# Kernel optimization log

Measured on AMD Instinct MI355X. Metric: run time of the kernel, lower is better.

## Reference

```python
import jax, jax.numpy as jnp
import numpy as np

B, S, E, L = 4, 4096, 64, 3
INIT_SCALE = 0.03


def setup_inputs() -> dict:
    key = jax.random.key(0)
    ks = jax.random.split(key, 7)
    return {
        "x": jax.random.normal(ks[0], (B, S, S + 1), dtype=jnp.float32),
        "q_ws": jax.random.normal(ks[1], (L, E, E), dtype=jnp.float32) * INIT_SCALE,
        "k_ws": jax.random.normal(ks[2], (L, E, E), dtype=jnp.float32) * INIT_SCALE,
        "v_ws": jax.random.normal(ks[3], (L, E, E), dtype=jnp.float32) * INIT_SCALE,
        "random_matrix": jax.random.normal(ks[4], (S, E - 1), dtype=jnp.float32) * INIT_SCALE,
        "coeffs_attended": jax.random.normal(ks[5], (S, E), dtype=jnp.float32) * INIT_SCALE,
        "offset": jax.random.normal(ks[6], (1,), dtype=jnp.float32),
    }


def reference(x, q_ws, k_ws, v_ws, random_matrix, coeffs_attended, offset):
    seq_length = random_matrix.shape[0]
    # project first seq_length feature columns, keep the last column raw -> [B, S, E]
    av = jnp.concatenate(
        [jnp.einsum('bsf,fe->bse', x[:, :, :seq_length], random_matrix), x[:, :, -1:]],
        axis=2,
    )

    def layer(av, ws):
        qw, kw, vw = ws
        q = jnp.einsum('bse,ed->bsd', av, qw)   # [B, S, E]
        k = jnp.einsum('bse,ed->bsd', av, kw)
        v = jnp.einsum('bse,ed->bsd', av, vw)
        scores = jax.nn.softmax(jnp.einsum('bqd,bkd->bqk', q, k), axis=-1)  # [B, S, S]
        out = jnp.einsum('bqk,bkd->bqd', scores, v)
        # skip_connections=False: output replaces attended values
        return out, None

    av, _ = jax.lax.scan(layer, av, (q_ws, k_ws, v_ws))
    final = jnp.einsum('bij,ij->b', av, coeffs_attended)  # [B]
    return final + offset[0]
```

## Files before the change

kernel.cpp:

```cpp
#include <hip/hip_runtime.h>

#define SEQ  4096
#define EMB  64
#define NB   4
#define XROW 4097

typedef unsigned short ushort_t;
typedef __attribute__((ext_vector_type(8))) short short8;
typedef __attribute__((ext_vector_type(4))) float floatx4;

__device__ __forceinline__ ushort_t f2bf(float f) {
    union { float f; unsigned int u; } v; v.f = f;
    unsigned int r = v.u + 0x7FFFu + ((v.u >> 16) & 1u);
    return (ushort_t)(r >> 16);
}

__global__ __launch_bounds__(256) void prep_rmt(const float* __restrict__ rm,
                                                ushort_t* __restrict__ rmT) {
    int o = (blockIdx.x * 256 + threadIdx.x) * 4;
    int e = o >> 12;
    int f = o & 4095;
    alignas(8) ushort_t t[4];
    t[0] = f2bf((e < 63) ? rm[(size_t)(f + 0) * 63 + e] : 0.f);
    t[1] = f2bf((e < 63) ? rm[(size_t)(f + 1) * 63 + e] : 0.f);
    t[2] = f2bf((e < 63) ? rm[(size_t)(f + 2) * 63 + e] : 0.f);
    t[3] = f2bf((e < 63) ? rm[(size_t)(f + 3) * 63 + e] : 0.f);
    *(uint2*)&rmT[o] = *(uint2*)t;
}

__global__ __launch_bounds__(256) void proj_mfma(const float* __restrict__ x,
        const ushort_t* __restrict__ rmT, float* __restrict__ av) {
    __shared__ ushort_t xs[64 * 64];
    __shared__ ushort_t rs[64 * 64];
    const int tid = threadIdx.x;
    const int row0 = blockIdx.x * 64;
    const int w = tid >> 6, l = tid & 63;
    const int srow = tid >> 2, sc = (tid & 3) * 16;

    floatx4 acc[4];
    #pragma unroll
    for (int i = 0; i < 4; ++i) acc[i] = (floatx4){0.f, 0.f, 0.f, 0.f};

    float px[16];
    short8 pr0, pr1;
    {
        const float* xp = x + (size_t)(row0 + srow) * XROW + sc;
        #pragma unroll
        for (int i = 0; i < 16; ++i) px[i] = xp[i];
        const ushort_t* rp = rmT + (size_t)srow * SEQ + sc;
        pr0 = *(const short8*)&rp[0];
        pr1 = *(const short8*)&rp[8];
    }

    for (int k0 = 0; k0 < SEQ; k0 += 64) {
        __syncthreads();
        {
            alignas(16) ushort_t tmp[16];
            #pragma unroll
            for (int i = 0; i < 16; ++i) tmp[i] = f2bf(px[i]);
            *(short8*)&xs[srow * 64 + sc]     = *(short8*)&tmp[0];
            *(short8*)&xs[srow * 64 + sc + 8] = *(short8*)&tmp[8];
            *(short8*)&rs[srow * 64 + sc]     = pr0;
            *(short8*)&rs[srow * 64 + sc + 8] = pr1;
        }
        __syncthreads();
        if (k0 + 64 < SEQ) {
            const float* xp = x + (size_t)(row0 + srow) * XROW + (k0 + 64) + sc;
            #pragma unroll
            for (int i = 0; i < 16; ++i) px[i] = xp[i];
            const ushort_t* rp = rmT + (size_t)srow * SEQ + (k0 + 64) + sc;
            pr0 = *(const short8*)&rp[0];
            pr1 = *(const short8*)&rp[8];
        }
        #pragma unroll
        for (int ksp = 0; ksp < 2; ++ksp) {
            short8 a = *(short8*)&xs[(w * 16 + (l & 15)) * 64 + ksp * 32 + (l >> 4) * 8];
            #pragma unroll
            for (int nt = 0; nt < 4; ++nt) {
                short8 bf = *(short8*)&rs[(nt * 16 + (l & 15)) * 64 + ksp * 32 + (l >> 4) * 8];
                acc[nt] = __builtin_amdgcn_mfma_f32_16x16x32_bf16(a, bf, acc[nt], 0, 0, 0);
            }
        }
    }
    #pragma unroll
    for (int nt = 0; nt < 4; ++nt)
        #pragma unroll
        for (int r = 0; r < 4; ++r) {
            int row = row0 + w * 16 + (l >> 4) * 4 + r;
            int col = nt * 16 + (l & 15);
            float v = acc[nt][r];
            if (col == 63) v = x[(size_t)row * XROW + SEQ];
            av[(size_t)row * EMB + col] = v;
        }
}

__global__ __launch_bounds__(256) void qkv_mfma(const float* __restrict__ av,
        const float* __restrict__ qw, const float* __restrict__ kw,
        const float* __restrict__ vw, ushort_t* __restrict__ Qb,
        ushort_t* __restrict__ Kb, ushort_t* __restrict__ Vt) {
    __shared__ ushort_t avs[64 * 64];
    __shared__ ushort_t wqs[64 * 64], wks[64 * 64], wvs[64 * 64];
    const int tid = threadIdx.x;
    const int row0 = blockIdx.x * 64;
    const int w = tid >> 6, l = tid & 63;
    const int srow = tid >> 2, sc = (tid & 3) * 16;

    {
        const float* ap = av + (size_t)(row0 + srow) * EMB + sc;
        alignas(16) ushort_t tmp[16];
        #pragma unroll
        for (int i = 0; i < 16; ++i) tmp[i] = f2bf(ap[i]);
        *(short8*)&avs[srow * 64 + sc]     = *(short8*)&tmp[0];
        *(short8*)&avs[srow * 64 + sc + 8] = *(short8*)&tmp[8];
    }
    {
        alignas(16) ushort_t tq[16], tk[16], tv[16];
        #pragma unroll
        for (int i = 0; i < 16; ++i) {
            int kk = sc + i;
            tq[i] = f2bf(qw[kk * 64 + srow]);
            tk[i] = f2bf(kw[kk * 64 + srow]);
            tv[i] = f2bf(vw[kk * 64 + srow]);
        }
        *(short8*)&wqs[srow * 64 + sc]     = *(short8*)&tq[0];
        *(short8*)&wqs[srow * 64 + sc + 8] = *(short8*)&tq[8];
        *(short8*)&wks[srow * 64 + sc]     = *(short8*)&tk[0];
        *(short8*)&wks[srow * 64 + sc + 8] = *(short8*)&tk[8];
        *(short8*)&wvs[srow * 64 + sc]     = *(short8*)&tv[0];
        *(short8*)&wvs[srow * 64 + sc + 8] = *(short8*)&tv[8];
    }
    __syncthreads();

    floatx4 aq[4], ak[4], avv[4];
    #pragma unroll
    for (int i = 0; i < 4; ++i) {
        aq[i] = (floatx4){0.f, 0.f, 0.f, 0.f};
        ak[i] = aq[i]; avv[i] = aq[i];
    }
    #pragma unroll
    for (int ksp = 0; ksp < 2; ++ksp) {
        short8 a = *(short8*)&avs[(w * 16 + (l & 15)) * 64 + ksp * 32 + (l >> 4) * 8];
        #pragma unroll
        for (int nt = 0; nt < 4; ++nt) {
            int bo = (nt * 16 + (l & 15)) * 64 + ksp * 32 + (l >> 4) * 8;
            aq[nt]  = __builtin_amdgcn_mfma_f32_16x16x32_bf16(a, *(short8*)&wqs[bo], aq[nt], 0, 0, 0);
            ak[nt]  = __builtin_amdgcn_mfma_f32_16x16x32_bf16(a, *(short8*)&wks[bo], ak[nt], 0, 0, 0);
            avv[nt] = __builtin_amdgcn_mfma_f32_16x16x32_bf16(a, *(short8*)&wvs[bo], avv[nt], 0, 0, 0);
        }
    }

    const int b = row0 >> 12;
    #pragma unroll
    for (int nt = 0; nt < 4; ++nt)
        #pragma unroll
        for (int r = 0; r < 4; ++r) {
            int row = row0 + w * 16 + (l >> 4) * 4 + r;
            int col = nt * 16 + (l & 15);
            size_t o = (size_t)row * EMB + col;
            Qb[o] = f2bf(aq[nt][r]);
            Kb[o] = f2bf(ak[nt][r]);
            Vt[((size_t)b * EMB + col) * SEQ + (row & 4095)] = f2bf(avv[nt][r]);
        }
}

__global__ __launch_bounds__(256) void flash_mfma(const ushort_t* __restrict__ Qb,
        const ushort_t* __restrict__ Kb, const ushort_t* __restrict__ Vt,
        float* __restrict__ out) {
    __shared__ ushort_t ks[64 * 64];
    __shared__ ushort_t vt[64 * 64];
    __shared__ ushort_t ps[4][16 * 64];
    const int tid = threadIdx.x;
    const int w = tid >> 6, l = tid & 63;
    const int b = blockIdx.y;
    const int q0 = blockIdx.x * 64;
    const size_t base  = (size_t)b * SEQ * EMB;
    const size_t vbase = (size_t)b * EMB * SEQ;
    const int srow = tid >> 2, sc = (tid & 3) * 16;

    short8 qf[2];
    #pragma unroll
    for (int ksp = 0; ksp < 2; ++ksp)
        qf[ksp] = *(const short8*)&Qb[base + (size_t)(q0 + w * 16 + (l & 15)) * EMB
                                      + ksp * 32 + (l >> 4) * 8];

    short8 pk0, pk1, pv0, pv1;
    {
        const ushort_t* kp = Kb + base + (size_t)srow * EMB + sc;
        pk0 = *(const short8*)kp;
        pk1 = *(const short8*)(kp + 8);
        const ushort_t* vp = Vt + vbase + (size_t)srow * SEQ + sc;
        pv0 = *(const short8*)vp;
        pv1 = *(const short8*)(vp + 8);
    }

    floatx4 o_acc[4];
    #pragma unroll
    for (int i = 0; i < 4; ++i) o_acc[i] = (floatx4){0.f, 0.f, 0.f, 0.f};
    float lpart[4] = {0.f, 0.f, 0.f, 0.f};

    for (int kt = 0; kt < SEQ; kt += 64) {
        __syncthreads();
        *(short8*)&ks[srow * 64 + sc]     = pk0;
        *(short8*)&ks[srow * 64 + sc + 8] = pk1;
        *(short8*)&vt[srow * 64 + sc]     = pv0;
        *(short8*)&vt[srow * 64 + sc + 8] = pv1;
        __syncthreads();
        if (kt + 64 < SEQ) {
            const ushort_t* kp = Kb + base + (size_t)(kt + 64 + srow) * EMB + sc;
            pk0 = *(const short8*)kp;
            pk1 = *(const short8*)(kp + 8);
            const ushort_t* vp = Vt + vbase + (size_t)srow * SEQ + (kt + 64) + sc;
            pv0 = *(const short8*)vp;
            pv1 = *(const short8*)(vp + 8);
        }

        floatx4 s[4];
        #pragma unroll
        for (int nt = 0; nt < 4; ++nt) s[nt] = (floatx4){0.f, 0.f, 0.f, 0.f};
        #pragma unroll
        for (int ksp = 0; ksp < 2; ++ksp)
            #pragma unroll
            for (int nt = 0; nt < 4; ++nt) {
                short8 bf = *(short8*)&ks[(nt * 16 + (l & 15)) * 64 + ksp * 32 + (l >> 4) * 8];
                s[nt] = __builtin_amdgcn_mfma_f32_16x16x32_bf16(qf[ksp], bf, s[nt], 0, 0, 0);
            }

        #pragma unroll
        for (int nt = 0; nt < 4; ++nt)
            #pragma unroll
            for (int r = 0; r < 4; ++r) {
                float p = __expf(s[nt][r]);
                lpart[r] += p;
                ps[w][((l >> 4) * 4 + r) * 64 + nt * 16 + (l & 15)] = f2bf(p);
            }
        asm volatile("s_waitcnt lgkmcnt(0)" ::: "memory");

        #pragma unroll
        for (int ksp = 0; ksp < 2; ++ksp) {
            short8 af = *(short8*)&ps[w][(l & 15) * 64 + ksp * 32 + (l >> 4) * 8];
            #pragma unroll
            for (int nt = 0; nt < 4; ++nt) {
                short8 bf = *(short8*)&vt[(nt * 16 + (l & 15)) * 64 + ksp * 32 + (l >> 4) * 8];
                o_acc[nt] = __builtin_amdgcn_mfma_f32_16x16x32_bf16(af, bf, o_acc[nt], 0, 0, 0);
            }
        }
    }

    #pragma unroll
    for (int r = 0; r < 4; ++r) {
        #pragma unroll
        for (int m = 1; m < 16; m <<= 1)
            lpart[r] += __shfl_xor(lpart[r], m);
        lpart[r] = 1.f / lpart[r];
    }
    #pragma unroll
    for (int nt = 0; nt < 4; ++nt)
        #pragma unroll
        for (int r = 0; r < 4; ++r) {
            int row = q0 + w * 16 + (l >> 4) * 4 + r;
            int col = nt * 16 + (l & 15);
            out[base + (size_t)row * EMB + col] = o_acc[nt][r] * lpart[r];
        }
}

__global__ void init_out(float* __restrict__ out, const float* __restrict__ offset) {
    if (threadIdx.x < NB) out[threadIdx.x] = offset[0];
}

__global__ __launch_bounds__(256) void reduce_kernel(const float* __restrict__ av,
        const float* __restrict__ coeffs, float* __restrict__ out) {
    const int b = blockIdx.y;
    const size_t base = (size_t)b * SEQ * EMB;
    const int local0 = blockIdx.x * 32768;
    const int tid = threadIdx.x;
    float ssum = 0.f;
    #pragma unroll 8
    for (int i = 0; i < 32; ++i) {
        int idx = local0 + (tid + i * 256) * 4;
        float4 a = *(const float4*)&av[base + idx];
        float4 c = *(const float4*)&coeffs[idx];
        ssum += a.x * c.x + a.y * c.y + a.z * c.z + a.w * c.w;
    }
    #pragma unroll
    for (int off = 1; off < 64; off <<= 1) ssum += __shfl_xor(ssum, off);
    __shared__ float wsum[4];
    if ((tid & 63) == 0) wsum[tid >> 6] = ssum;
    __syncthreads();
    if (tid == 0)
        atomicAdd(&out[b], wsum[0] + wsum[1] + wsum[2] + wsum[3]);
}

extern "C" void kernel_launch(void* const* d_in, const int* in_sizes, int n_in,
                              void* d_out, int out_size, void* d_ws, size_t ws_size,
                              hipStream_t stream) {
    const float* x      = (const float*)d_in[0];
    const float* q_ws   = (const float*)d_in[1];
    const float* k_ws   = (const float*)d_in[2];
    const float* v_ws   = (const float*)d_in[3];
    const float* rm     = (const float*)d_in[4];
    const float* coeffs = (const float*)d_in[5];
    const float* offset = (const float*)d_in[6];
    float* out = (float*)d_out;
    char* ws = (char*)d_ws;

    float*    AV  = (float*)ws;
    ushort_t* Qb  = (ushort_t*)(ws + 4 * 1024 * 1024);
    ushort_t* Kb  = (ushort_t*)(ws + 6 * 1024 * 1024);
    ushort_t* Vt  = (ushort_t*)(ws + 8 * 1024 * 1024);
    ushort_t* rmT = (ushort_t*)(ws + 10 * 1024 * 1024);

    prep_rmt<<<256, 256, 0, stream>>>(rm, rmT);
    proj_mfma<<<256, 256, 0, stream>>>(x, rmT, AV);
    for (int layer = 0; layer < 3; ++layer) {
        qkv_mfma<<<256, 256, 0, stream>>>(AV, q_ws + layer * 4096,
                                          k_ws + layer * 4096, v_ws + layer * 4096,
                                          Qb, Kb, Vt);
        flash_mfma<<<dim3(64, NB), 256, 0, stream>>>(Qb, Kb, Vt, AV);
    }
    init_out<<<1, 64, 0, stream>>>(out, offset);
    reduce_kernel<<<dim3(8, NB), 256, 0, stream>>>(AV, coeffs, out);
}
```

Before: 623.8 us.

## Split K dimension across two wave groups in projection and flash attention

Projection and attention kernels now run 512 threads per block. Two groups of four waves each process half of the key/feature dimension and merge their partial accumulators and row sums through LDS at the end. This doubles the waves per block to hide latency, since only 256 blocks were launched before. The flash kernel also swaps MFMA operand order so each lane holds a full 4-element P row segment, then writes P to LDS with a swizzled, packed layout to cut bank conflicts. The init kernel is folded into prep_rmt and the reduce grid is doubled, at the cost of extra LDS and an added merge step.

Result: faster. 570.7 us (-8.5%).

```diff
diff --git a/kernel.cpp b/kernel.cpp
--- a/kernel.cpp
+++ b/kernel.cpp
@@ -9,14 +9,25 @@
 typedef __attribute__((ext_vector_type(8))) short short8;
 typedef __attribute__((ext_vector_type(4))) float floatx4;
 
+union U8 { uint4 u; short8 s8; };
+
 __device__ __forceinline__ ushort_t f2bf(float f) {
     union { float f; unsigned int u; } v; v.f = f;
     unsigned int r = v.u + 0x7FFFu + ((v.u >> 16) & 1u);
     return (ushort_t)(r >> 16);
 }
+__device__ __forceinline__ uint2 pack4bf(float a, float b, float c, float d) {
+    uint2 p;
+    p.x = (unsigned)f2bf(a) | ((unsigned)f2bf(b) << 16);
+    p.y = (unsigned)f2bf(c) | ((unsigned)f2bf(d) << 16);
+    return p;
+}
 
 __global__ __launch_bounds__(256) void prep_rmt(const float* __restrict__ rm,
-                                                ushort_t* __restrict__ rmT) {
+                                                ushort_t* __restrict__ rmT,
+                                                float* __restrict__ out,
+                                                const float* __restrict__ offset) {
+    if (blockIdx.x == 0 && threadIdx.x < NB) out[threadIdx.x] = offset[0];
     int o = (blockIdx.x * 256 + threadIdx.x) * 4;
     int e = o >> 12;
     int f = o & 4095;
@@ -28,14 +39,19 @@
     *(uint2*)&rmT[o] = *(uint2*)t;
 }
 
-__global__ __launch_bounds__(256) void proj_mfma(const float* __restrict__ x,
+__global__ __launch_bounds__(512) void proj_mfma(const float* __restrict__ x,
         const ushort_t* __restrict__ rmT, float* __restrict__ av) {
-    __shared__ ushort_t xs[64 * 64];
-    __shared__ ushort_t rs[64 * 64];
+    __shared__ ushort_t xs[2][64 * 64];
+    __shared__ ushort_t rs[2][64 * 64];
     const int tid = threadIdx.x;
     const int row0 = blockIdx.x * 64;
     const int w = tid >> 6, l = tid & 63;
-    const int srow = tid >> 2, sc = (tid & 3) * 16;
+    const int wg = w >> 2;
+    const int wq = w & 3;
+    const int t4 = tid & 255;
+    const int srow = t4 >> 2, sc = (t4 & 3) * 16;
+    const int kbase = wg * 2048;
+    const int quad = l >> 4, q16 = l & 15;
 
     floatx4 acc[4];
     #pragma unroll
@@ -44,54 +60,67 @@
     float px[16];
     short8 pr0, pr1;
     {
-        const float* xp = x + (size_t)(row0 + srow) * XROW + sc;
+        const float* xp = x + (size_t)(row0 + srow) * XROW + kbase + sc;
         #pragma unroll
         for (int i = 0; i < 16; ++i) px[i] = xp[i];
-        const ushort_t* rp = rmT + (size_t)srow * SEQ + sc;
+        const ushort_t* rp = rmT + (size_t)srow * SEQ + kbase + sc;
         pr0 = *(const short8*)&rp[0];
         pr1 = *(const short8*)&rp[8];
     }
 
-    for (int k0 = 0; k0 < SEQ; k0 += 64) {
+    for (int k0 = 0; k0 < 2048; k0 += 64) {
         __syncthreads();
         {
             alignas(16) ushort_t tmp[16];
             #pragma unroll
             for (int i = 0; i < 16; ++i) tmp[i] = f2bf(px[i]);
-            *(short8*)&xs[srow * 64 + sc]     = *(short8*)&tmp[0];
-            *(short8*)&xs[srow * 64 + sc + 8] = *(short8*)&tmp[8];
-            *(short8*)&rs[srow * 64 + sc]     = pr0;
-            *(short8*)&rs[srow * 64 + sc + 8] = pr1;
+            *(short8*)&xs[wg][srow * 64 + sc]     = *(short8*)&tmp[0];
+            *(short8*)&xs[wg][srow * 64 + sc + 8] = *(short8*)&tmp[8];
+            *(short8*)&rs[wg][srow * 64 + sc]     = pr0;
+            *(short8*)&rs[wg][srow * 64 + sc + 8] = pr1;
         }
         __syncthreads();
-        if (k0 + 64 < SEQ) {
-            const float* xp = x + (size_t)(row0 + srow) * XROW + (k0 + 64) + sc;
+        if (k0 + 64 < 2048) {
+            const float* xp = x + (size_t)(row0 + srow) * XROW + kbase + k0 + 64 + sc;
             #pragma unroll
             for (int i = 0; i < 16; ++i) px[i] = xp[i];
-            const ushort_t* rp = rmT + (size_t)srow * SEQ + (k0 + 64) + sc;
+            const ushort_t* rp = rmT + (size_t)srow * SEQ + kbase + k0 + 64 + sc;
             pr0 = *(const short8*)&rp[0];
             pr1 = *(const short8*)&rp[8];
         }
         #pragma unroll
         for (int ksp = 0; ksp < 2; ++ksp) {
-            short8 a = *(short8*)&xs[(w * 16 + (l & 15)) * 64 + ksp * 32 + (l >> 4) * 8];
+            short8 a = *(short8*)&xs[wg][(wq * 16 + q16) * 64 + ksp * 32 + quad * 8];
             #pragma unroll
             for (int nt = 0; nt < 4; ++nt) {
-                short8 bf = *(short8*)&rs[(nt * 16 + (l & 15)) * 64 + ksp * 32 + (l >> 4) * 8];
+                short8 bf = *(short8*)&rs[wg][(nt * 16 + q16) * 64 + ksp * 32 + quad * 8];
                 acc[nt] = __builtin_amdgcn_mfma_f32_16x16x32_bf16(a, bf, acc[nt], 0, 0, 0);
             }
         }
     }
-    #pragma unroll
-    for (int nt = 0; nt < 4; ++nt)
-        #pragma unroll
-        for (int r = 0; r < 4; ++r) {
-            int row = row0 + w * 16 + (l >> 4) * 4 + r;
-            int col = nt * 16 + (l & 15);
-            float v = acc[nt][r];
-            if (col == 63) v = x[(size_t)row * XROW + SEQ];
-            av[(size_t)row * EMB + col] = v;
-        }
+
+    __syncthreads();
+    float* poc = (float*)xs;
+    if (wg == 1) {
+        #pragma unroll
+        for (int nt = 0; nt < 4; ++nt)
+            #pragma unroll
+            for (int r = 0; r < 4; ++r)
+                poc[(wq * 16 + quad * 4 + r) * 64 + nt * 16 + q16] = acc[nt][r];
+    }
+    __syncthreads();
+    if (wg == 0) {
+        #pragma unroll
+        for (int nt = 0; nt < 4; ++nt)
+            #pragma unroll
+            for (int r = 0; r < 4; ++r) {
+                int row = row0 + wq * 16 + quad * 4 + r;
+                int col = nt * 16 + q16;
+                float v = acc[nt][r] + poc[(wq * 16 + quad * 4 + r) * 64 + col];
+                if (col == 63) v = x[(size_t)row * XROW + SEQ];
+                av[(size_t)row * EMB + col] = v;
+            }
+    }
 }
 
 __global__ __launch_bounds__(256) void qkv_mfma(const float* __restrict__ av,
@@ -163,32 +192,38 @@
         }
 }
 
-__global__ __launch_bounds__(256) void flash_mfma(const ushort_t* __restrict__ Qb,
+__global__ __launch_bounds__(512) void flash_mfma(const ushort_t* __restrict__ Qb,
         const ushort_t* __restrict__ Kb, const ushort_t* __restrict__ Vt,
         float* __restrict__ out) {
-    __shared__ ushort_t ks[64 * 64];
-    __shared__ ushort_t vt[64 * 64];
-    __shared__ ushort_t ps[4][16 * 64];
+    __shared__ ushort_t ks[2][64 * 64];
+    __shared__ ushort_t vt[2][64 * 64];
+    __shared__ ushort_t psbuf[8 * 1024];
+    __shared__ float lrow[2][64];
     const int tid = threadIdx.x;
     const int w = tid >> 6, l = tid & 63;
+    const int wg = w >> 2, wq = w & 3;
+    const int quad = l >> 4, q16 = l & 15;
     const int b = blockIdx.y;
     const int q0 = blockIdx.x * 64;
     const size_t base  = (size_t)b * SEQ * EMB;
     const size_t vbase = (size_t)b * EMB * SEQ;
-    const int srow = tid >> 2, sc = (tid & 3) * 16;
+    const int t4 = tid & 255;
+    const int srow = t4 >> 2, sc = (t4 & 3) * 16;
+    const int kbase = wg * 2048;
+    ushort_t* ps = &psbuf[w * 1024];
 
     short8 qf[2];
     #pragma unroll
     for (int ksp = 0; ksp < 2; ++ksp)
-        qf[ksp] = *(const short8*)&Qb[base + (size_t)(q0 + w * 16 + (l & 15)) * EMB
-                                      + ksp * 32 + (l >> 4) * 8];
+        qf[ksp] = *(const short8*)&Qb[base + (size_t)(q0 + wq * 16 + q16) * EMB
+                                      + ksp * 32 + quad * 8];
 
     short8 pk0, pk1, pv0, pv1;
     {
-        const ushort_t* kp = Kb + base + (size_t)srow * EMB + sc;
+        const ushort_t* kp = Kb + base + (size_t)(kbase + srow) * EMB + sc;
         pk0 = *(const short8*)kp;
         pk1 = *(const short8*)(kp + 8);
-        const ushort_t* vp = Vt + vbase + (size_t)srow * SEQ + sc;
+        const ushort_t* vp = Vt + vbase + (size_t)srow * SEQ + kbase + sc;
         pv0 = *(const short8*)vp;
         pv1 = *(const short8*)(vp + 8);
     }
@@ -196,20 +231,20 @@
     floatx4 o_acc[4];
     #pragma unroll
     for (int i = 0; i < 4; ++i) o_acc[i] = (floatx4){0.f, 0.f, 0.f, 0.f};
-    float lpart[4] = {0.f, 0.f, 0.f, 0.f};
-
-    for (int kt = 0; kt < SEQ; kt += 64) {
+    float lpart = 0.f;
+
+    for (int kt0 = 0; kt0 < 2048; kt0 += 64) {
         __syncthreads();
-        *(short8*)&ks[srow * 64 + sc]     = pk0;
-        *(short8*)&ks[srow * 64 + sc + 8] = pk1;
-        *(short8*)&vt[srow * 64 + sc]     = pv0;
-        *(short8*)&vt[srow * 64 + sc + 8] = pv1;
+        *(short8*)&ks[wg][srow * 64 + sc]     = pk0;
+        *(short8*)&ks[wg][srow * 64 + sc + 8] = pk1;
+        *(short8*)&vt[wg][srow * 64 + sc]     = pv0;
+        *(short8*)&vt[wg][srow * 64 + sc + 8] = pv1;
         __syncthreads();
-        if (kt + 64 < SEQ) {
-            const ushort_t* kp = Kb + base + (size_t)(kt + 64 + srow) * EMB + sc;
+        if (kt0 + 64 < 2048) {
+            const ushort_t* kp = Kb + base + (size_t)(kbase + kt0 + 64 + srow) * EMB + sc;
             pk0 = *(const short8*)kp;
             pk1 = *(const short8*)(kp + 8);
-            const ushort_t* vp = Vt + vbase + (size_t)srow * SEQ + (kt + 64) + sc;
+            const ushort_t* vp = Vt + vbase + (size_t)srow * SEQ + kbase + kt0 + 64 + sc;
             pv0 = *(const short8*)vp;
             pv1 = *(const short8*)(vp + 8);
         }
@@ -221,61 +256,78 @@
         for (int ksp = 0; ksp < 2; ++ksp)
             #pragma unroll
             for (int nt = 0; nt < 4; ++nt) {
-                short8 bf = *(short8*)&ks[(nt * 16 + (l & 15)) * 64 + ksp * 32 + (l >> 4) * 8];
-                s[nt] = __builtin_amdgcn_mfma_f32_16x16x32_bf16(qf[ksp], bf, s[nt], 0, 0, 0);
-            }
-
+                short8 a = *(short8*)&ks[wg][(nt * 16 + q16) * 64 + ksp * 32 + quad * 8];
+                s[nt] = __builtin_amdgcn_mfma_f32_16x16x32_bf16(a, qf[ksp], s[nt], 0, 0, 0);
+            }
+
+        #pragma unroll
+        for (int nt = 0; nt < 4; ++nt) {
+            float p0 = __expf(s[nt][0]);
+            float p1 = __expf(s[nt][1]);
+            float p2 = __expf(s[nt][2]);
+            float p3 = __expf(s[nt][3]);
+            lpart += (p0 + p1) + (p2 + p3);
+            int g = nt * 4 + quad;
+            *(uint2*)&ps[q16 * 64 + ((g ^ q16) & 15) * 4] = pack4bf(p0, p1, p2, p3);
+        }
+        asm volatile("s_waitcnt lgkmcnt(0)" ::: "memory");
+
+        #pragma unroll
+        for (int ksp = 0; ksp < 2; ++ksp) {
+            int g0 = ksp * 8 + quad * 2;
+            uint2 a0 = *(uint2*)&ps[q16 * 64 + ((g0 ^ q16) & 15) * 4];
+            uint2 a1 = *(uint2*)&ps[q16 * 64 + (((g0 + 1) ^ q16) & 15) * 4];
+            U8 af;
+            af.u.x = a0.x; af.u.y = a0.y; af.u.z = a1.x; af.u.w = a1.y;
+            #pragma unroll
+            for (int nt = 0; nt < 4; ++nt) {
+                short8 bf = *(short8*)&vt[wg][(nt * 16 + q16) * 64 + ksp * 32 + quad * 8];
+                o_acc[nt] = __builtin_amdgcn_mfma_f32_16x16x32_bf16(af.s8, bf, o_acc[nt], 0, 0, 0);
+            }
+        }
+    }
+
+    lpart += __shfl_xor(lpart, 16);
+    lpart += __shfl_xor(lpart, 32);
+    __syncthreads();
+    if (quad == 0) lrow[wg][wq * 16 + q16] = lpart;
+    float* oc = (float*)psbuf;
+    if (wg == 1) {
         #pragma unroll
         for (int nt = 0; nt < 4; ++nt)
             #pragma unroll
+            for (int r = 0; r < 4; ++r)
+                oc[(wq * 16 + quad * 4 + r) * 64 + nt * 16 + q16] = o_acc[nt][r];
+    }
+    __syncthreads();
+    if (wg == 0) {
+        float linv[4];
+        #pragma unroll
+        for (int r = 0; r < 4; ++r) {
+            int q = wq * 16 + quad * 4 + r;
+            linv[r] = 1.f / (lrow[0][q] + lrow[1][q]);
+        }
+        #pragma unroll
+        for (int nt = 0; nt < 4; ++nt)
+            #pragma unroll
             for (int r = 0; r < 4; ++r) {
-                float p = __expf(s[nt][r]);
-                lpart[r] += p;
-                ps[w][((l >> 4) * 4 + r) * 64 + nt * 16 + (l & 15)] = f2bf(p);
-            }
-        asm volatile("s_waitcnt lgkmcnt(0)" ::: "memory");
-
-        #pragma unroll
-        for (int ksp = 0; ksp < 2; ++ksp) {
-            short8 af = *(short8*)&ps[w][(l & 15) * 64 + ksp * 32 + (l >> 4) * 8];
-            #pragma unroll
-            for (int nt = 0; nt < 4; ++nt) {
-                short8 bf = *(short8*)&vt[(nt * 16 + (l & 15)) * 64 + ksp * 32 + (l >> 4) * 8];
-                o_acc[nt] = __builtin_amdgcn_mfma_f32_16x16x32_bf16(af, bf, o_acc[nt], 0, 0, 0);
-            }
-        }
-    }
-
-    #pragma unroll
-    for (int r = 0; r < 4; ++r) {
-        #pragma unroll
-        for (int m = 1; m < 16; m <<= 1)
-            lpart[r] += __shfl_xor(lpart[r], m);
-        lpart[r] = 1.f / lpart[r];
-    }
-    #pragma unroll
-    for (int nt = 0; nt < 4; ++nt)
-        #pragma unroll
-        for (int r = 0; r < 4; ++r) {
-            int row = q0 + w * 16 + (l >> 4) * 4 + r;
-            int col = nt * 16 + (l & 15);
-            out[base + (size_t)row * EMB + col] = o_acc[nt][r] * lpart[r];
-        }
-}
-
-__global__ void init_out(float* __restrict__ out, const float* __restrict__ offset) {
-    if (threadIdx.x < NB) out[threadIdx.x] = offset[0];
+                int row = q0 + wq * 16 + quad * 4 + r;
+                int col = nt * 16 + q16;
+                float v = (o_acc[nt][r] + oc[(wq * 16 + quad * 4 + r) * 64 + col]) * linv[r];
+                out[base + (size_t)row * EMB + col] = v;
+            }
+    }
 }
 
 __global__ __launch_bounds__(256) void reduce_kernel(const float* __restrict__ av,
         const float* __restrict__ coeffs, float* __restrict__ out) {
     const int b = blockIdx.y;
     const size_t base = (size_t)b * SEQ * EMB;
-    const int local0 = blockIdx.x * 32768;
+    const int local0 = blockIdx.x * 16384;
     const int tid = threadIdx.x;
     float ssum = 0.f;
     #pragma unroll 8
-    for (int i = 0; i < 32; ++i) {
+    for (int i = 0; i < 16; ++i) {
         int idx = local0 + (tid + i * 256) * 4;
         float4 a = *(const float4*)&av[base + idx];
         float4 c = *(const float4*)&coeffs[idx];
@@ -309,14 +361,13 @@
     ushort_t* Vt  = (ushort_t*)(ws + 8 * 1024 * 1024);
     ushort_t* rmT = (ushort_t*)(ws + 10 * 1024 * 1024);
 
-    prep_rmt<<<256, 256, 0, stream>>>(rm, rmT);
-    proj_mfma<<<256, 256, 0, stream>>>(x, rmT, AV);
+    prep_rmt<<<256, 256, 0, stream>>>(rm, rmT, out, offset);
+    proj_mfma<<<256, 512, 0, stream>>>(x, rmT, AV);
     for (int layer = 0; layer < 3; ++layer) {
         qkv_mfma<<<256, 256, 0, stream>>>(AV, q_ws + layer * 4096,
                                           k_ws + layer * 4096, v_ws + layer * 4096,
                                           Qb, Kb, Vt);
-        flash_mfma<<<dim3(64, NB), 256, 0, stream>>>(Qb, Kb, Vt, AV);
-    }
-    init_out<<<1, 64, 0, stream>>>(out, offset);
-    reduce_kernel<<<dim3(8, NB), 256, 0, stream>>>(AV, coeffs, out);
-}
+        flash_mfma<<<dim3(64, NB), 512, 0, stream>>>(Qb, Kb, Vt, AV);
+    }
+    reduce_kernel<<<dim3(16, NB), 256, 0, stream>>>(AV, coeffs, out);
+}
```
